# Kernel tuning notes

Measured on AMD Instinct MI355X. Metric: run time of the kernel, lower is better.

Reference implementation:

```python
import jax, jax.numpy as jnp
import numpy as np

B, H, W, C = 4, 64, 64, 256
D = C // 8  # q/k projection dim


def setup_inputs() -> dict:
    key = jax.random.key(0)
    ks = jax.random.split(key, 5)
    scale = lambda fan_in: 1.0 / np.sqrt(fan_in)
    return {
        "x": jax.random.normal(ks[0], (B, H, W, C), dtype=jnp.float32),
        "wq": jax.random.normal(ks[1], (C, D), dtype=jnp.float32) * scale(C),
        "bq": jnp.zeros((D,), dtype=jnp.float32),
        "wk": jax.random.normal(ks[2], (C, D), dtype=jnp.float32) * scale(C),
        "bk": jnp.zeros((D,), dtype=jnp.float32),
        "wv": jax.random.normal(ks[3], (C, C), dtype=jnp.float32) * scale(C),
        "bv": jnp.zeros((C,), dtype=jnp.float32),
        "wo": jax.random.normal(ks[4], (C, C), dtype=jnp.float32) * scale(C),
        "bo": jnp.zeros((C,), dtype=jnp.float32),
    }


def reference(x, wq, bq, wk, bk, wv, bv, wo, bo):
    b, h, w, c = x.shape
    n = h * w
    xt = x.reshape(b, n, c)  # 1x1 conv == per-pixel linear over channels
    q = xt @ wq + bq                      # [b, n, d]
    k = xt @ wk + bk                      # [b, n, d]
    v = xt @ wv + bv                      # [b, n, c]
    scores = jnp.einsum("bnd,bmd->bnm", q, k) / jnp.sqrt(jnp.float32(k.shape[-1]))
    attn = jax.nn.softmax(scores, axis=-1)  # [b, n, n]
    attended = jnp.einsum("bnm,bmc->bnc", attn, v)  # [b, n, c]
    out = attended @ wo + bo
    return x + out.reshape(b, h, w, c)
```

## Files before the change

kernel.cpp:

```cpp
#include <hip/hip_runtime.h>
#include <math.h>

#define B_   4
#define N_   4096
#define C_   256
#define D_   32

typedef __attribute__((ext_vector_type(8))) short short8;
typedef __attribute__((ext_vector_type(4))) float f32x4;
typedef __attribute__((ext_vector_type(4))) unsigned short us4;

__device__ __forceinline__ unsigned short f2bf(float f) {
    unsigned int u = __float_as_uint(f);
    u = (u + 0x7FFFu + ((u >> 16) & 1u)) >> 16;
    return (unsigned short)u;
}
__device__ __forceinline__ unsigned short p2bf(float f) {
    return (unsigned short)((__float_as_uint(f) + 0x8000u) >> 16);
}
__device__ __forceinline__ float bf2f(unsigned short h) {
    return __uint_as_float(((unsigned int)h) << 16);
}

__device__ __forceinline__ void dma16(const unsigned short* g, unsigned short* l) {
    __builtin_amdgcn_global_load_lds(
        (const __attribute__((address_space(1))) unsigned int*)(uintptr_t)(g),
        (__attribute__((address_space(3))) unsigned int*)(unsigned int)(uintptr_t)(l),
        16, 0, 0);
}

__global__ __launch_bounds__(256) void prep_w_kernel(const float* __restrict__ wq,
                                                     const float* __restrict__ wk,
                                                     const float* __restrict__ wv,
                                                     const float* __restrict__ wo,
                                                     unsigned short* __restrict__ wqkvT,
                                                     unsigned short* __restrict__ woT) {
    int idx = blockIdx.x * 256 + threadIdx.x;
    if (idx < 320 * 256) {
        int n = idx >> 8, c = idx & 255;
        float v = (n < 32) ? wq[c * 32 + n]
                : (n < 64) ? wk[c * 32 + (n - 32)]
                           : wv[c * 256 + (n - 64)];
        wqkvT[idx] = f2bf(v);
    } else {
        int j = idx - 320 * 256;
        int n = j >> 8, c = j & 255;
        woT[j] = f2bf(wo[c * 256 + n]);
    }
}

__global__ __launch_bounds__(256) void qkv_gemm_kernel(const float* __restrict__ x,
        const unsigned short* __restrict__ wqkvT,
        const float* __restrict__ bq, const float* __restrict__ bk, const float* __restrict__ bv,
        unsigned short* __restrict__ qb, unsigned short* __restrict__ kb,
        unsigned short* __restrict__ vT) {
    const int tid = threadIdx.x;
    const int wave = tid >> 6, lane = tid & 63;
    const int quad = lane >> 4, li = lane & 15;
    const int rows0 = blockIdx.x * 32;
    const float kS = 0.17677669529663687f * 1.4426950408889634f;

    __shared__ __align__(16) unsigned short xs[32 * 264];

#pragma unroll
    for (int i = 0; i < 8; ++i) {
        int flat = i * 256 + tid;
        int row = flat >> 6, c4 = flat & 63;
        float4 f = *(const float4*)(x + (size_t)(rows0 + row) * 256 + c4 * 4);
        us4 o = { f2bf(f.x), f2bf(f.y), f2bf(f.z), f2bf(f.w) };
        *(us4*)&xs[row * 264 + c4 * 4] = o;
    }
    __syncthreads();

    const int rowt = wave & 1;
    const int nt0 = (wave >> 1) * 10;
    const int r0 = rows0 + rowt * 16;

    short8 A[8];
#pragma unroll
    for (int kc = 0; kc < 8; ++kc)
        A[kc] = *(const short8*)&xs[(rowt * 16 + li) * 264 + kc * 32 + quad * 8];

#pragma unroll
    for (int j = 0; j < 10; ++j) {
        const int nt = nt0 + j;
        f32x4 acc = {0.f, 0.f, 0.f, 0.f};
#pragma unroll
        for (int kc = 0; kc < 8; ++kc) {
            short8 Bf = *(const short8*)(wqkvT + (size_t)(nt * 16 + li) * 256 + kc * 32 + quad * 8);
            acc = __builtin_amdgcn_mfma_f32_16x16x32_bf16(A[kc], Bf, acc, 0, 0, 0);
        }
        int n = nt * 16 + li;
        float bias = (nt < 2) ? bq[n] : (nt < 4) ? bk[n - 32] : bv[n - 64];
        if (nt < 4) {
            unsigned short* dst = (nt < 2) ? qb : kb;
            float scl = (nt < 2) ? kS : 1.0f;
            int d = (nt < 2) ? n : (n - 32);
#pragma unroll
            for (int jj = 0; jj < 4; ++jj)
                dst[(size_t)(r0 + quad * 4 + jj) * 32 + d] = f2bf((acc[jj] + bias) * scl);
        } else {
            int c = n - 64;
            int p = r0 + quad * 4;
            int b = p >> 12, ni = p & 4095;
            us4 hv = { f2bf(acc[0] + bias), f2bf(acc[1] + bias),
                       f2bf(acc[2] + bias), f2bf(acc[3] + bias) };
            *(us4*)(vT + ((size_t)(b * 256 + c) * 4096 + ni)) = hv;
        }
    }
}

__global__ __launch_bounds__(256, 2) void attn_partial_kernel(
        const unsigned short* __restrict__ qb, const unsigned short* __restrict__ kb,
        const unsigned short* __restrict__ vT,
        unsigned short* __restrict__ Obf, float* __restrict__ ml) {
    const int tid = threadIdx.x;
    const int wave = tid >> 6, lane = tid & 63;
    const int quad = lane >> 4, li = lane & 15;

    const int bid = blockIdx.x;
    const int xcd = bid & 7, jj_ = bid >> 3;
    const int qt = jj_ & 31;
    const int g = (xcd << 1) | (jj_ >> 5);
    const int by = g >> 2, sg = g & 3;
    const int pw = qt * 128 + wave * 32;
    const int key0 = sg * 1024;

    __shared__ __align__(16) unsigned short smem[29696];
    unsigned short* pw_ = smem + 24576 + wave * 1280;

    short8 a_q[2];
#pragma unroll
    for (int qf = 0; qf < 2; ++qf)
        a_q[qf] = *(const short8*)(qb + (size_t)(by * N_ + pw + qf * 16 + li) * 32 + quad * 8);

    const int o8 = lane >> 3, s8 = lane & 7;
    const int sp = s8 ^ o8;
    const int chl = sp >> 2, chk = sp & 3;
    auto stage = [&](int kt, unsigned short* buf) {
#pragma unroll
        for (int h = 0; h < 4; ++h) {
            int ch = ((h * 32 + wave * 8 + o8) << 1) + chl;
            const unsigned short* g2 = vT + (size_t)(by * 256 + ch) * 4096
                                         + key0 + kt * 32 + chk * 8;
            dma16(g2, buf + (h * 256 + wave * 64) * 8);
        }
    };

    stage(0, smem);
    short8 kf0, kf1;
    {
        const unsigned short* krow = kb + (size_t)(by * N_ + key0) * 32;
        kf0 = *(const short8*)(krow + li * 32 + quad * 8);
        kf1 = *(const short8*)(krow + (16 + li) * 32 + quad * 8);
    }
    stage(1, smem + 8192);

    const f32x4 Z = {0.f, 0.f, 0.f, 0.f};
    f32x4 O[2][16];
#pragma unroll
    for (int qf = 0; qf < 2; ++qf)
#pragma unroll
        for (int ct = 0; ct < 16; ++ct) O[qf][ct] = Z;
    f32x4 lsum[2] = {Z, Z};
    short8 ones;
#pragma unroll
    for (int j = 0; j < 8; ++j) ones[j] = (short)0x3F80;

    const int voff = (li >> 1) * 64 + ((((li & 1) * 4 + quad) ^ ((li >> 1) & 7)) * 8);

    unsigned short* vc  = smem;
    unsigned short* vn1 = smem + 8192;
    unsigned short* vn2 = smem + 16384;
#pragma unroll 1
    for (int kt = 0; kt < 32; ++kt) {
        if (kt == 0)      asm volatile("s_waitcnt vmcnt(4)" ::: "memory");
        else if (kt < 31) asm volatile("s_waitcnt vmcnt(6)" ::: "memory");
        else              asm volatile("s_waitcnt vmcnt(2)" ::: "memory");
        __builtin_amdgcn_s_barrier();

        short8 kn0 = kf0, kn1 = kf1;
        if (kt < 31) {
            const unsigned short* krow = kb + (size_t)(by * N_ + key0 + (kt + 1) * 32) * 32;
            kn0 = *(const short8*)(krow + li * 32 + quad * 8);
            kn1 = *(const short8*)(krow + (16 + li) * 32 + quad * 8);
        }
        if (kt < 30) stage(kt + 2, vn2);

#pragma unroll
        for (int qf = 0; qf < 2; ++qf) {
            f32x4 s0 = __builtin_amdgcn_mfma_f32_16x16x32_bf16(a_q[qf], kf0, Z, 0, 0, 0);
            f32x4 s1 = __builtin_amdgcn_mfma_f32_16x16x32_bf16(a_q[qf], kf1, Z, 0, 0, 0);
#pragma unroll
            for (int r = 0; r < 4; ++r) {
                float p0 = __builtin_amdgcn_exp2f(s0[r]);
                float p1 = __builtin_amdgcn_exp2f(s1[r]);
                pw_[(qf * 16 + quad * 4 + r) * 40 + li]      = p2bf(p0);
                pw_[(qf * 16 + quad * 4 + r) * 40 + 16 + li] = p2bf(p1);
            }
        }

        short8 ap0 = *(const short8*)(pw_ + li * 40 + quad * 8);
        short8 ap1 = *(const short8*)(pw_ + (16 + li) * 40 + quad * 8);
        __builtin_amdgcn_s_setprio(1);
        lsum[0] = __builtin_amdgcn_mfma_f32_16x16x32_bf16(ap0, ones, lsum[0], 0, 0, 0);
        lsum[1] = __builtin_amdgcn_mfma_f32_16x16x32_bf16(ap1, ones, lsum[1], 0, 0, 0);
#pragma unroll
        for (int ct = 0; ct < 16; ++ct) {
            short8 bv8 = *(const short8*)(vc + ct * 512 + voff);
            O[0][ct] = __builtin_amdgcn_mfma_f32_16x16x32_bf16(ap0, bv8, O[0][ct], 0, 0, 0);
            O[1][ct] = __builtin_amdgcn_mfma_f32_16x16x32_bf16(ap1, bv8, O[1][ct], 0, 0, 0);
        }
        __builtin_amdgcn_s_setprio(0);

        kf0 = kn0; kf1 = kn1;
        unsigned short* t = vc; vc = vn1; vn1 = vn2; vn2 = t;
    }

    __syncthreads();
    unsigned short* att = smem + wave * 4224;
    const int srow = lane & 15, scc = (lane >> 4) * 64;
#pragma unroll
    for (int qf = 0; qf < 2; ++qf) {
#pragma unroll
        for (int ct = 0; ct < 16; ++ct)
#pragma unroll
            for (int r = 0; r < 4; ++r)
                att[(quad * 4 + r) * 264 + ct * 16 + li] = f2bf(O[qf][ct][r]);
        const int pbase = by * N_ + pw + qf * 16;
        unsigned short* dst = Obf + ((size_t)(pbase + srow) * 4 + sg) * 256 + scc;
#pragma unroll
        for (int h = 0; h < 8; ++h)
            *(short8*)(dst + h * 8) = *(const short8*)(att + srow * 264 + scc + h * 8);
        if (li == 0) {
#pragma unroll
            for (int r = 0; r < 4; ++r) {
                int pp = pbase + quad * 4 + r;
                ml[pp * 4 + sg] = lsum[qf][r];
            }
        }
    }
}

__global__ __launch_bounds__(256) void merge_proj_kernel(
        const unsigned short* __restrict__ Obf, const float* __restrict__ ml,
        const unsigned short* __restrict__ woT, const float* __restrict__ x,
        const float* __restrict__ bo, float* __restrict__ out) {
    const int tid = threadIdx.x;
    const int px = blockIdx.x * 16;
    __shared__ __align__(16) unsigned short att[16 * 264];

    {
        const int row = tid >> 4, chc = tid & 15;
        const int p = px + row;
        float lt = ml[p * 4] + ml[p * 4 + 1] + ml[p * 4 + 2] + ml[p * 4 + 3];
        float inv = 1.0f / lt;
        float acc[16];
#pragma unroll
        for (int i = 0; i < 16; ++i) acc[i] = 0.f;
#pragma unroll
        for (int s = 0; s < 4; ++s) {
            const unsigned short* src = Obf + (size_t)(p * 4 + s) * 256 + chc * 16;
            short8 v0 = *(const short8*)(src);
            short8 v1 = *(const short8*)(src + 8);
#pragma unroll
            for (int jj = 0; jj < 8; ++jj) {
                acc[jj]     += bf2f((unsigned short)v0[jj]);
                acc[8 + jj] += bf2f((unsigned short)v1[jj]);
            }
        }
        short8 o0, o1;
#pragma unroll
        for (int jj = 0; jj < 8; ++jj) {
            o0[jj] = (short)f2bf(acc[jj] * inv);
            o1[jj] = (short)f2bf(acc[8 + jj] * inv);
        }
        *(short8*)&att[row * 264 + chc * 16]     = o0;
        *(short8*)&att[row * 264 + chc * 16 + 8] = o1;
    }
    __syncthreads();

    const int wave = tid >> 6, lane = tid & 63;
    const int quad = lane >> 4, li = lane & 15;
    short8 bfr[8];
#pragma unroll
    for (int kc = 0; kc < 8; ++kc)
        bfr[kc] = *(const short8*)&att[li * 264 + kc * 32 + quad * 8];
#pragma unroll
    for (int mt = 0; mt < 4; ++mt) {
        const int mtg = wave * 4 + mt;
        f32x4 acc = {0.f, 0.f, 0.f, 0.f};
#pragma unroll
        for (int kc = 0; kc < 8; ++kc) {
            short8 aw = *(const short8*)(woT + (size_t)(mtg * 16 + li) * 256 + kc * 32 + quad * 8);
            acc = __builtin_amdgcn_mfma_f32_16x16x32_bf16(aw, bfr[kc], acc, 0, 0, 0);
        }
        const int pg = px + li;
        const float4 xv  = *(const float4*)(x  + (size_t)pg * 256 + mtg * 16 + quad * 4);
        const float4 bv4 = *(const float4*)(bo + mtg * 16 + quad * 4);
        float4 o4;
        o4.x = acc[0] + xv.x + bv4.x;
        o4.y = acc[1] + xv.y + bv4.y;
        o4.z = acc[2] + xv.z + bv4.z;
        o4.w = acc[3] + xv.w + bv4.w;
        *(float4*)(out + (size_t)pg * 256 + mtg * 16 + quad * 4) = o4;
    }
}

extern "C" void kernel_launch(void* const* d_in, const int* in_sizes, int n_in,
                              void* d_out, int out_size, void* d_ws, size_t ws_size,
                              hipStream_t stream) {
    const float* x  = (const float*)d_in[0];
    const float* wq = (const float*)d_in[1];
    const float* bq = (const float*)d_in[2];
    const float* wk = (const float*)d_in[3];
    const float* bk = (const float*)d_in[4];
    const float* wv = (const float*)d_in[5];
    const float* bv = (const float*)d_in[6];
    const float* wo = (const float*)d_in[7];
    const float* bo = (const float*)d_in[8];
    float* out = (float*)d_out;

    char* ws = (char*)d_ws;
    unsigned short* wqkvT = (unsigned short*)(ws);
    unsigned short* woT   = (unsigned short*)(ws +   163840);
    unsigned short* qb    = (unsigned short*)(ws +   294912);
    unsigned short* kb    = (unsigned short*)(ws +  1343488);
    unsigned short* vT    = (unsigned short*)(ws +  2392064);
    unsigned short* Obf   = (unsigned short*)(ws + 10780672);
    float*          ml    = (float*)         (ws + 44335104);

    hipLaunchKernelGGL(prep_w_kernel,      dim3(576),       dim3(256), 0, stream, wq, wk, wv, wo, wqkvT, woT);
    hipLaunchKernelGGL(qkv_gemm_kernel,    dim3(512),       dim3(256), 0, stream, x, wqkvT, bq, bk, bv, qb, kb, vT);
    hipLaunchKernelGGL(attn_partial_kernel,dim3(512),       dim3(256), 0, stream, qb, kb, vT, Obf, ml);
    hipLaunchKernelGGL(merge_proj_kernel,  dim3(1024),      dim3(256), 0, stream, Obf, ml, woT, x, bo, out);
}
```

Before: 177.4 us.

## Share P tiles across waves and split PV accumulation by channel

Each wave now writes its exponentiated scores to shared memory, and after a barrier every wave multiplies all 128 query rows by its own 64-channel slice of V. This cuts per-wave V reads from LDS and shrinks redundant V fragment loads. The cost is an extra barrier per key tile and more P reads. Row sums move from MFMA-with-ones to scalar accumulation followed by a cross-lane shuffle reduction, and the epilogue is restructured into two passes through shared memory.

```diff
diff --git a/kernel.cpp b/kernel.cpp
--- a/kernel.cpp
+++ b/kernel.cpp
@@ -123,16 +123,18 @@
     const int qt = jj_ & 31;
     const int g = (xcd << 1) | (jj_ >> 5);
     const int by = g >> 2, sg = g & 3;
-    const int pw = qt * 128 + wave * 32;
+    const int pwb = qt * 128;
+    const int q0w = pwb + wave * 32;
     const int key0 = sg * 1024;
 
     __shared__ __align__(16) unsigned short smem[29696];
-    unsigned short* pw_ = smem + 24576 + wave * 1280;
+    unsigned short* pw_all = smem + 24576;
+    unsigned short* pw_own = pw_all + wave * 1280;
 
     short8 a_q[2];
 #pragma unroll
     for (int qf = 0; qf < 2; ++qf)
-        a_q[qf] = *(const short8*)(qb + (size_t)(by * N_ + pw + qf * 16 + li) * 32 + quad * 8);
+        a_q[qf] = *(const short8*)(qb + (size_t)(by * N_ + q0w + qf * 16 + li) * 32 + quad * 8);
 
     const int o8 = lane >> 3, s8 = lane & 7;
     const int sp = s8 ^ o8;
@@ -157,15 +159,12 @@
     stage(1, smem + 8192);
 
     const f32x4 Z = {0.f, 0.f, 0.f, 0.f};
-    f32x4 O[2][16];
-#pragma unroll
-    for (int qf = 0; qf < 2; ++qf)
-#pragma unroll
-        for (int ct = 0; ct < 16; ++ct) O[qf][ct] = Z;
-    f32x4 lsum[2] = {Z, Z};
-    short8 ones;
-#pragma unroll
-    for (int j = 0; j < 8; ++j) ones[j] = (short)0x3F80;
+    f32x4 O[8][4];
+#pragma unroll
+    for (int qf = 0; qf < 8; ++qf)
+#pragma unroll
+        for (int ct = 0; ct < 4; ++ct) O[qf][ct] = Z;
+    float lsum_s[2][4] = {{0.f,0.f,0.f,0.f},{0.f,0.f,0.f,0.f}};
 
     const int voff = (li >> 1) * 64 + ((((li & 1) * 4 + quad) ^ ((li >> 1) & 7)) * 8);
 
@@ -195,50 +194,75 @@
             for (int r = 0; r < 4; ++r) {
                 float p0 = __builtin_amdgcn_exp2f(s0[r]);
                 float p1 = __builtin_amdgcn_exp2f(s1[r]);
-                pw_[(qf * 16 + quad * 4 + r) * 40 + li]      = p2bf(p0);
-                pw_[(qf * 16 + quad * 4 + r) * 40 + 16 + li] = p2bf(p1);
+                unsigned short b0 = p2bf(p0), b1 = p2bf(p1);
+                pw_own[(qf * 16 + quad * 4 + r) * 40 + li]      = b0;
+                pw_own[(qf * 16 + quad * 4 + r) * 40 + 16 + li] = b1;
+                lsum_s[qf][r] += bf2f(b0) + bf2f(b1);
             }
         }
 
-        short8 ap0 = *(const short8*)(pw_ + li * 40 + quad * 8);
-        short8 ap1 = *(const short8*)(pw_ + (16 + li) * 40 + quad * 8);
-        __builtin_amdgcn_s_setprio(1);
-        lsum[0] = __builtin_amdgcn_mfma_f32_16x16x32_bf16(ap0, ones, lsum[0], 0, 0, 0);
-        lsum[1] = __builtin_amdgcn_mfma_f32_16x16x32_bf16(ap1, ones, lsum[1], 0, 0, 0);
-#pragma unroll
-        for (int ct = 0; ct < 16; ++ct) {
-            short8 bv8 = *(const short8*)(vc + ct * 512 + voff);
-            O[0][ct] = __builtin_amdgcn_mfma_f32_16x16x32_bf16(ap0, bv8, O[0][ct], 0, 0, 0);
-            O[1][ct] = __builtin_amdgcn_mfma_f32_16x16x32_bf16(ap1, bv8, O[1][ct], 0, 0, 0);
-        }
-        __builtin_amdgcn_s_setprio(0);
+        asm volatile("s_waitcnt lgkmcnt(0)" ::: "memory");
+        __builtin_amdgcn_s_barrier();
+
+        short8 ap0_, ap1_, ap2_, ap3_, ap4_, ap5_, ap6_, ap7_;
+        ap0_ = *(const short8*)(pw_all + 0 * 1280 + li * 40 + quad * 8);
+        ap1_ = *(const short8*)(pw_all + 0 * 1280 + (16 + li) * 40 + quad * 8);
+        ap2_ = *(const short8*)(pw_all + 1 * 1280 + li * 40 + quad * 8);
+        ap3_ = *(const short8*)(pw_all + 1 * 1280 + (16 + li) * 40 + quad * 8);
+        ap4_ = *(const short8*)(pw_all + 2 * 1280 + li * 40 + quad * 8);
+        ap5_ = *(const short8*)(pw_all + 2 * 1280 + (16 + li) * 40 + quad * 8);
+        ap6_ = *(const short8*)(pw_all + 3 * 1280 + li * 40 + quad * 8);
+        ap7_ = *(const short8*)(pw_all + 3 * 1280 + (16 + li) * 40 + quad * 8);
+#pragma unroll
+        for (int ct = 0; ct < 4; ++ct) {
+            short8 bv8 = *(const short8*)(vc + (wave * 4 + ct) * 512 + voff);
+            O[0][ct] = __builtin_amdgcn_mfma_f32_16x16x32_bf16(ap0_, bv8, O[0][ct], 0, 0, 0);
+            O[1][ct] = __builtin_amdgcn_mfma_f32_16x16x32_bf16(ap1_, bv8, O[1][ct], 0, 0, 0);
+            O[2][ct] = __builtin_amdgcn_mfma_f32_16x16x32_bf16(ap2_, bv8, O[2][ct], 0, 0, 0);
+            O[3][ct] = __builtin_amdgcn_mfma_f32_16x16x32_bf16(ap3_, bv8, O[3][ct], 0, 0, 0);
+            O[4][ct] = __builtin_amdgcn_mfma_f32_16x16x32_bf16(ap4_, bv8, O[4][ct], 0, 0, 0);
+            O[5][ct] = __builtin_amdgcn_mfma_f32_16x16x32_bf16(ap5_, bv8, O[5][ct], 0, 0, 0);
+            O[6][ct] = __builtin_amdgcn_mfma_f32_16x16x32_bf16(ap6_, bv8, O[6][ct], 0, 0, 0);
+            O[7][ct] = __builtin_amdgcn_mfma_f32_16x16x32_bf16(ap7_, bv8, O[7][ct], 0, 0, 0);
+        }
 
         kf0 = kn0; kf1 = kn1;
         unsigned short* t = vc; vc = vn1; vn1 = vn2; vn2 = t;
     }
 
-    __syncthreads();
-    unsigned short* att = smem + wave * 4224;
+#pragma unroll
+    for (int h = 0; h < 2; ++h)
+#pragma unroll
+        for (int r = 0; r < 4; ++r) {
+            float v = lsum_s[h][r];
+            v += __shfl_xor(v, 1);
+            v += __shfl_xor(v, 2);
+            v += __shfl_xor(v, 4);
+            v += __shfl_xor(v, 8);
+            if (li == 0)
+                ml[(size_t)(by * N_ + q0w + h * 16 + quad * 4 + r) * 4 + sg] = v;
+        }
+
+    unsigned short* att = smem;
     const int srow = lane & 15, scc = (lane >> 4) * 64;
 #pragma unroll
-    for (int qf = 0; qf < 2; ++qf) {
-#pragma unroll
-        for (int ct = 0; ct < 16; ++ct)
-#pragma unroll
-            for (int r = 0; r < 4; ++r)
-                att[(quad * 4 + r) * 264 + ct * 16 + li] = f2bf(O[qf][ct][r]);
-        const int pbase = by * N_ + pw + qf * 16;
-        unsigned short* dst = Obf + ((size_t)(pbase + srow) * 4 + sg) * 256 + scc;
+    for (int pass = 0; pass < 2; ++pass) {
+        __syncthreads();
+#pragma unroll
+        for (int qf = 0; qf < 4; ++qf)
+#pragma unroll
+            for (int ct = 0; ct < 4; ++ct)
+#pragma unroll
+                for (int r = 0; r < 4; ++r)
+                    att[(qf * 16 + quad * 4 + r) * 264 + wave * 64 + ct * 16 + li] =
+                        f2bf(O[pass * 4 + qf][ct][r]);
+        __syncthreads();
+        const int p = pwb + pass * 64 + wave * 16 + srow;
+        unsigned short* dst = Obf + ((size_t)(by * N_ + p) * 4 + sg) * 256 + scc;
+        const unsigned short* srcr = att + (wave * 16 + srow) * 264 + scc;
 #pragma unroll
         for (int h = 0; h < 8; ++h)
-            *(short8*)(dst + h * 8) = *(const short8*)(att + srow * 264 + scc + h * 8);
-        if (li == 0) {
-#pragma unroll
-            for (int r = 0; r < 4; ++r) {
-                int pp = pbase + quad * 4 + r;
-                ml[pp * 4 + sg] = lsum[qf][r];
-            }
-        }
+            *(short8*)(dst + h * 8) = *(const short8*)(srcr + h * 8);
     }
 }
 
```

Result: no change. 180.8 us (+1.9%).

## Software-pipeline QK^T/exp of next tile ahead of PV MFMAs with double-buffered P

Applied to the files above, without the earlier changes.

Restructures the attention inner loop so the scores and exp for key tile kt+1 are computed and written to a second LDS P buffer while the PV MFMAs for tile kt use P fragments already in registers. K fragments are prefetched two tiles ahead, and a prologue computes the first P tile before the loop. The aim is to overlap the exp/VALU and LDS round-trip with matrix work instead of serialising them. It costs extra LDS (which may affect occupancy), more live registers for the prefetched K fragments and held P fragments, and it drops the setprio hints.

```diff
diff --git a/kernel.cpp b/kernel.cpp
--- a/kernel.cpp
+++ b/kernel.cpp
@@ -126,8 +126,9 @@
     const int pw = qt * 128 + wave * 32;
     const int key0 = sg * 1024;
 
-    __shared__ __align__(16) unsigned short smem[29696];
-    unsigned short* pw_ = smem + 24576 + wave * 1280;
+    __shared__ __align__(16) unsigned short smem[34816];
+    unsigned short* pA = smem + 24576 + wave * 2560;
+    unsigned short* pB = pA + 1280;
 
     short8 a_q[2];
 #pragma unroll
@@ -148,13 +149,18 @@
     };
 
     stage(0, smem);
-    short8 kf0, kf1;
+    short8 kc0, kc1, kn0, kn1;
     {
         const unsigned short* krow = kb + (size_t)(by * N_ + key0) * 32;
-        kf0 = *(const short8*)(krow + li * 32 + quad * 8);
-        kf1 = *(const short8*)(krow + (16 + li) * 32 + quad * 8);
+        kc0 = *(const short8*)(krow + li * 32 + quad * 8);
+        kc1 = *(const short8*)(krow + (16 + li) * 32 + quad * 8);
     }
     stage(1, smem + 8192);
+    {
+        const unsigned short* krow = kb + (size_t)(by * N_ + key0 + 32) * 32;
+        kn0 = *(const short8*)(krow + li * 32 + quad * 8);
+        kn1 = *(const short8*)(krow + (16 + li) * 32 + quad * 8);
+    }
 
     const f32x4 Z = {0.f, 0.f, 0.f, 0.f};
     f32x4 O[2][16];
@@ -166,6 +172,21 @@
     short8 ones;
 #pragma unroll
     for (int j = 0; j < 8; ++j) ones[j] = (short)0x3F80;
+
+#pragma unroll
+    for (int qf = 0; qf < 2; ++qf) {
+        f32x4 s0 = __builtin_amdgcn_mfma_f32_16x16x32_bf16(a_q[qf], kc0, Z, 0, 0, 0);
+        f32x4 s1 = __builtin_amdgcn_mfma_f32_16x16x32_bf16(a_q[qf], kc1, Z, 0, 0, 0);
+#pragma unroll
+        for (int r = 0; r < 4; ++r) {
+            pA[(qf * 16 + quad * 4 + r) * 40 + li]      = p2bf(__builtin_amdgcn_exp2f(s0[r]));
+            pA[(qf * 16 + quad * 4 + r) * 40 + 16 + li] = p2bf(__builtin_amdgcn_exp2f(s1[r]));
+        }
+    }
+    short8 ap0 = *(const short8*)(pA + li * 40 + quad * 8);
+    short8 ap1 = *(const short8*)(pA + (16 + li) * 40 + quad * 8);
+    kc0 = kn0; kc1 = kn1;
+    unsigned short* wr = pB;
 
     const int voff = (li >> 1) * 64 + ((((li & 1) * 4 + quad) ^ ((li >> 1) & 7)) * 8);
 
@@ -174,35 +195,30 @@
     unsigned short* vn2 = smem + 16384;
 #pragma unroll 1
     for (int kt = 0; kt < 32; ++kt) {
-        if (kt == 0)      asm volatile("s_waitcnt vmcnt(4)" ::: "memory");
-        else if (kt < 31) asm volatile("s_waitcnt vmcnt(6)" ::: "memory");
-        else              asm volatile("s_waitcnt vmcnt(2)" ::: "memory");
+        if (kt < 31) asm volatile("s_waitcnt vmcnt(6)" ::: "memory");
+        else         asm volatile("s_waitcnt vmcnt(0)" ::: "memory");
         __builtin_amdgcn_s_barrier();
 
-        short8 kn0 = kf0, kn1 = kf1;
-        if (kt < 31) {
-            const unsigned short* krow = kb + (size_t)(by * N_ + key0 + (kt + 1) * 32) * 32;
+        if (kt <= 29) {
+            stage(kt + 2, vn2);
+            const unsigned short* krow = kb + (size_t)(by * N_ + key0 + (kt + 2) * 32) * 32;
             kn0 = *(const short8*)(krow + li * 32 + quad * 8);
             kn1 = *(const short8*)(krow + (16 + li) * 32 + quad * 8);
         }
-        if (kt < 30) stage(kt + 2, vn2);
-
-#pragma unroll
-        for (int qf = 0; qf < 2; ++qf) {
-            f32x4 s0 = __builtin_amdgcn_mfma_f32_16x16x32_bf16(a_q[qf], kf0, Z, 0, 0, 0);
-            f32x4 s1 = __builtin_amdgcn_mfma_f32_16x16x32_bf16(a_q[qf], kf1, Z, 0, 0, 0);
-#pragma unroll
-            for (int r = 0; r < 4; ++r) {
-                float p0 = __builtin_amdgcn_exp2f(s0[r]);
-                float p1 = __builtin_amdgcn_exp2f(s1[r]);
-                pw_[(qf * 16 + quad * 4 + r) * 40 + li]      = p2bf(p0);
-                pw_[(qf * 16 + quad * 4 + r) * 40 + 16 + li] = p2bf(p1);
+
+        if (kt <= 30) {
+#pragma unroll
+            for (int qf = 0; qf < 2; ++qf) {
+                f32x4 s0 = __builtin_amdgcn_mfma_f32_16x16x32_bf16(a_q[qf], kc0, Z, 0, 0, 0);
+                f32x4 s1 = __builtin_amdgcn_mfma_f32_16x16x32_bf16(a_q[qf], kc1, Z, 0, 0, 0);
+#pragma unroll
+                for (int r = 0; r < 4; ++r) {
+                    wr[(qf * 16 + quad * 4 + r) * 40 + li]      = p2bf(__builtin_amdgcn_exp2f(s0[r]));
+                    wr[(qf * 16 + quad * 4 + r) * 40 + 16 + li] = p2bf(__builtin_amdgcn_exp2f(s1[r]));
+                }
             }
         }
 
-        short8 ap0 = *(const short8*)(pw_ + li * 40 + quad * 8);
-        short8 ap1 = *(const short8*)(pw_ + (16 + li) * 40 + quad * 8);
-        __builtin_amdgcn_s_setprio(1);
         lsum[0] = __builtin_amdgcn_mfma_f32_16x16x32_bf16(ap0, ones, lsum[0], 0, 0, 0);
         lsum[1] = __builtin_amdgcn_mfma_f32_16x16x32_bf16(ap1, ones, lsum[1], 0, 0, 0);
 #pragma unroll
@@ -211,9 +227,13 @@
             O[0][ct] = __builtin_amdgcn_mfma_f32_16x16x32_bf16(ap0, bv8, O[0][ct], 0, 0, 0);
             O[1][ct] = __builtin_amdgcn_mfma_f32_16x16x32_bf16(ap1, bv8, O[1][ct], 0, 0, 0);
         }
-        __builtin_amdgcn_s_setprio(0);
-
-        kf0 = kn0; kf1 = kn1;
+
+        if (kt <= 30) {
+            ap0 = *(const short8*)(wr + li * 40 + quad * 8);
+            ap1 = *(const short8*)(wr + (16 + li) * 40 + quad * 8);
+            wr = (wr == pA) ? pB : pA;
+        }
+        kc0 = kn0; kc1 = kn1;
         unsigned short* t = vc; vc = vn1; vn1 = vn2; vn2 = t;
     }
 
```

Result: no change. 179.0 us (+0.9%).

## Load V tiles directly from global into registers instead of LDS staging

Applied to the files above, without the earlier changes.

Replaces the triple-buffered global-to-LDS DMA staging of V (with waitcnt/barrier sync) with per-lane direct global loads into a rotating 8-entry register buffer, prefetched one step ahead inside the MFMA loop. This removes the per-iteration block barrier and LDS traffic and shrinks shared memory. The risks are exposed global-load latency, since each prefetch is only one MFMA group ahead, less coalesced 16-byte reads per lane, and extra VGPR pressure at two waves per SIMD.

```diff
diff --git a/kernel.cpp b/kernel.cpp
--- a/kernel.cpp
+++ b/kernel.cpp
@@ -20,13 +20,6 @@
 }
 __device__ __forceinline__ float bf2f(unsigned short h) {
     return __uint_as_float(((unsigned int)h) << 16);
-}
-
-__device__ __forceinline__ void dma16(const unsigned short* g, unsigned short* l) {
-    __builtin_amdgcn_global_load_lds(
-        (const __attribute__((address_space(1))) unsigned int*)(uintptr_t)(g),
-        (__attribute__((address_space(3))) unsigned int*)(unsigned int)(uintptr_t)(l),
-        16, 0, 0);
 }
 
 __global__ __launch_bounds__(256) void prep_w_kernel(const float* __restrict__ wq,
@@ -126,35 +119,27 @@
     const int pw = qt * 128 + wave * 32;
     const int key0 = sg * 1024;
 
-    __shared__ __align__(16) unsigned short smem[29696];
-    unsigned short* pw_ = smem + 24576 + wave * 1280;
+    __shared__ __align__(16) unsigned short smem[16896];
+    unsigned short* pw_ = smem + wave * 1280;
 
     short8 a_q[2];
 #pragma unroll
     for (int qf = 0; qf < 2; ++qf)
         a_q[qf] = *(const short8*)(qb + (size_t)(by * N_ + pw + qf * 16 + li) * 32 + quad * 8);
 
-    const int o8 = lane >> 3, s8 = lane & 7;
-    const int sp = s8 ^ o8;
-    const int chl = sp >> 2, chk = sp & 3;
-    auto stage = [&](int kt, unsigned short* buf) {
-#pragma unroll
-        for (int h = 0; h < 4; ++h) {
-            int ch = ((h * 32 + wave * 8 + o8) << 1) + chl;
-            const unsigned short* g2 = vT + (size_t)(by * 256 + ch) * 4096
-                                         + key0 + kt * 32 + chk * 8;
-            dma16(g2, buf + (h * 256 + wave * 64) * 8);
-        }
-    };
-
-    stage(0, smem);
-    short8 kf0, kf1;
+    short8 kc0, kc1, kn0, kn1;
     {
         const unsigned short* krow = kb + (size_t)(by * N_ + key0) * 32;
-        kf0 = *(const short8*)(krow + li * 32 + quad * 8);
-        kf1 = *(const short8*)(krow + (16 + li) * 32 + quad * 8);
-    }
-    stage(1, smem + 8192);
+        kc0 = *(const short8*)(krow + li * 32 + quad * 8);
+        kc1 = *(const short8*)(krow + (16 + li) * 32 + quad * 8);
+    }
+
+    const unsigned short* vrow = vT + (size_t)(by * 256 + li) * 4096 + key0 + quad * 8;
+
+    short8 vb[8];
+#pragma unroll
+    for (int j = 0; j < 8; ++j)
+        vb[j] = *(const short8*)(vrow + (size_t)j * 16 * 4096);
 
     const f32x4 Z = {0.f, 0.f, 0.f, 0.f};
     f32x4 O[2][16];
@@ -167,30 +152,20 @@
 #pragma unroll
     for (int j = 0; j < 8; ++j) ones[j] = (short)0x3F80;
 
-    const int voff = (li >> 1) * 64 + ((((li & 1) * 4 + quad) ^ ((li >> 1) & 7)) * 8);
-
-    unsigned short* vc  = smem;
-    unsigned short* vn1 = smem + 8192;
-    unsigned short* vn2 = smem + 16384;
 #pragma unroll 1
     for (int kt = 0; kt < 32; ++kt) {
-        if (kt == 0)      asm volatile("s_waitcnt vmcnt(4)" ::: "memory");
-        else if (kt < 31) asm volatile("s_waitcnt vmcnt(6)" ::: "memory");
-        else              asm volatile("s_waitcnt vmcnt(2)" ::: "memory");
-        __builtin_amdgcn_s_barrier();
-
-        short8 kn0 = kf0, kn1 = kf1;
-        if (kt < 31) {
-            const unsigned short* krow = kb + (size_t)(by * N_ + key0 + (kt + 1) * 32) * 32;
+        const int ktn = (kt < 31) ? kt + 1 : kt;
+
+        {
+            const unsigned short* krow = kb + (size_t)(by * N_ + key0 + ktn * 32) * 32;
             kn0 = *(const short8*)(krow + li * 32 + quad * 8);
             kn1 = *(const short8*)(krow + (16 + li) * 32 + quad * 8);
         }
-        if (kt < 30) stage(kt + 2, vn2);
 
 #pragma unroll
         for (int qf = 0; qf < 2; ++qf) {
-            f32x4 s0 = __builtin_amdgcn_mfma_f32_16x16x32_bf16(a_q[qf], kf0, Z, 0, 0, 0);
-            f32x4 s1 = __builtin_amdgcn_mfma_f32_16x16x32_bf16(a_q[qf], kf1, Z, 0, 0, 0);
+            f32x4 s0 = __builtin_amdgcn_mfma_f32_16x16x32_bf16(a_q[qf], kc0, Z, 0, 0, 0);
+            f32x4 s1 = __builtin_amdgcn_mfma_f32_16x16x32_bf16(a_q[qf], kc1, Z, 0, 0, 0);
 #pragma unroll
             for (int r = 0; r < 4; ++r) {
                 float p0 = __builtin_amdgcn_exp2f(s0[r]);
@@ -199,22 +174,21 @@
                 pw_[(qf * 16 + quad * 4 + r) * 40 + 16 + li] = p2bf(p1);
             }
         }
-
         short8 ap0 = *(const short8*)(pw_ + li * 40 + quad * 8);
         short8 ap1 = *(const short8*)(pw_ + (16 + li) * 40 + quad * 8);
-        __builtin_amdgcn_s_setprio(1);
+
         lsum[0] = __builtin_amdgcn_mfma_f32_16x16x32_bf16(ap0, ones, lsum[0], 0, 0, 0);
         lsum[1] = __builtin_amdgcn_mfma_f32_16x16x32_bf16(ap1, ones, lsum[1], 0, 0, 0);
 #pragma unroll
         for (int ct = 0; ct < 16; ++ct) {
-            short8 bv8 = *(const short8*)(vc + ct * 512 + voff);
-            O[0][ct] = __builtin_amdgcn_mfma_f32_16x16x32_bf16(ap0, bv8, O[0][ct], 0, 0, 0);
-            O[1][ct] = __builtin_amdgcn_mfma_f32_16x16x32_bf16(ap1, bv8, O[1][ct], 0, 0, 0);
-        }
-        __builtin_amdgcn_s_setprio(0);
-
-        kf0 = kn0; kf1 = kn1;
-        unsigned short* t = vc; vc = vn1; vn1 = vn2; vn2 = t;
+            O[0][ct] = __builtin_amdgcn_mfma_f32_16x16x32_bf16(ap0, vb[ct & 7], O[0][ct], 0, 0, 0);
+            O[1][ct] = __builtin_amdgcn_mfma_f32_16x16x32_bf16(ap1, vb[ct & 7], O[1][ct], 0, 0, 0);
+            const int nct = (ct < 8) ? ct + 8 : ct - 8;
+            const int nkt = (ct < 8) ? kt : ktn;
+            vb[ct & 7] = *(const short8*)(vrow + (size_t)nct * 16 * 4096 + nkt * 32);
+        }
+
+        kc0 = kn0; kc1 = kn1;
     }
 
     __syncthreads();
```

Result: slower. 259.2 us (+46.2%).
